# Optimization experiments

Measured on AMD Instinct MI355X. Metric: run time of the kernel, lower is better.

## Reference

```python
import jax, jax.numpy as jnp
import numpy as np

B, T, D = 4, 2048, 768
D_CONV, D_GRIF, D_FFN, K = 384, 384, 2048, 3
EPS = 1e-6


def rmsnorm(x, w):
    rms = jax.lax.rsqrt(jnp.mean(jnp.square(x.astype(jnp.float32)), axis=-1, keepdims=True) + EPS)
    return (x.astype(jnp.float32) * rms).astype(x.dtype) * w


def causal_dwconv(x, w):
    # x: [B,T,C], w: [C,K] depthwise causal conv
    k = w.shape[1]
    xp = jnp.pad(x, ((0, 0), (k - 1, 0), (0, 0)))  # left pad -> causal
    out = jax.lax.conv_general_dilated(
        xp.transpose(0, 2, 1), w[:, None, :],  # [B,C,T+K-1], [C,1,K]
        window_strides=(1,), padding='VALID',
        dimension_numbers=('NCW', 'OIW', 'NCW'),
        feature_group_count=w.shape[0])
    return out.transpose(0, 2, 1)  # [B,T,C]


def rg_lru(v, r, i, lam):
    # Griffin RG-LRU: log_a = -8*softplus(lam)*r; h_t = a*h_{t-1} + sqrt(1-a^2)*(i*v)
    log_a = -8.0 * jax.nn.softplus(lam) * r                # [B,T,Dg]
    a = jnp.exp(log_a)
    gated = jnp.sqrt(jnp.maximum(1.0 - jnp.exp(2.0 * log_a), EPS)) * (i * v)
    def comb(c1, c2):
        a1, b1 = c1
        a2, b2 = c2
        return (a1 * a2, a2 * b1 + b2)
    _, h = jax.lax.associative_scan(comb, (a, gated), axis=1)
    return h


def setup_inputs() -> dict:
    key = jax.random.key(0)
    ks = jax.random.split(key, 16)
    s_in = 1.0 / np.sqrt(D)
    s_ffn = 1.0 / np.sqrt(D_FFN)
    return {
        'x': jax.random.normal(ks[0], (B, T, D), jnp.float32),
        'velocity': jnp.zeros((B, T, D), jnp.float32),
        'pre_norm_w': jnp.ones((D,), jnp.float32),
        'conv_in_w': jax.random.normal(ks[1], (D, 2 * D_CONV), jnp.float32) * s_in,
        'conv_dw_w': jax.random.normal(ks[2], (D_CONV, K), jnp.float32) * (1.0 / np.sqrt(K)),
        'grif_v_w': jax.random.normal(ks[3], (D, D_GRIF), jnp.float32) * s_in,
        'grif_r_w': jax.random.normal(ks[4], (D, D_GRIF), jnp.float32) * s_in,
        'grif_i_w': jax.random.normal(ks[5], (D, D_GRIF), jnp.float32) * s_in,
        'grif_lam': jax.random.uniform(ks[6], (D_GRIF,), jnp.float32, 0.5, 2.0),
        'out_w': jax.random.normal(ks[7], (D, D), jnp.float32) * s_in,
        'log_beta': jnp.array(0.0, jnp.float32),  # log(0.5/(1-0.5))
        'ffn_norm_w': jnp.ones((D,), jnp.float32),
        'w1': jax.random.normal(ks[8], (D, D_FFN), jnp.float32) * s_in,
        'w3': jax.random.normal(ks[9], (D, D_FFN), jnp.float32) * s_in,
        'w2': jax.random.normal(ks[10], (D_FFN, D), jnp.float32) * s_ffn,
    }


def reference(x, velocity, pre_norm_w, conv_in_w, conv_dw_w, grif_v_w, grif_r_w,
              grif_i_w, grif_lam, out_w, log_beta, ffn_norm_w, w1, w3, w2):
    xn = rmsnorm(x, pre_norm_w)
    # GatedConv branch -> [B,T,D_CONV]
    u, g = jnp.split(xn @ conv_in_w, 2, axis=-1)
    conv_out = causal_dwconv(u, conv_dw_w) * jax.nn.silu(g)
    # Griffin RG-LRU branch -> [B,T,D_GRIF]
    v = xn @ grif_v_w
    r = jax.nn.sigmoid(xn @ grif_r_w)
    i = jax.nn.sigmoid(xn @ grif_i_w)
    griffin_out = rg_lru(v, r, i, grif_lam)
    # concat -> out_proj -> momentum residual
    mixer_out = jnp.concatenate([conv_out, griffin_out], axis=-1) @ out_w
    beta = jax.nn.sigmoid(log_beta)
    velocity = beta * velocity + mixer_out
    x = x + velocity
    # ffn: RMSNorm -> SwiGLU -> residual
    normed = rmsnorm(x, ffn_norm_w)
    x = x + (jax.nn.silu(normed @ w1) * (normed @ w3)) @ w2
    return (x, velocity)
```

## Files before the change

kernel.cpp:

```cpp
#include <hip/hip_runtime.h>
#include <hip/hip_bf16.h>
#include <cstdint>

#define BSZ   4
#define TSEQ  2048
#define DMOD  768
#define DCONV 384
#define DGRIF 384
#define DFFN  2048
#define BT    (BSZ*TSEQ)
#define NG1   1920
#define EPS_  1e-6f

typedef __bf16 bf16;
typedef __bf16 bf16x8 __attribute__((ext_vector_type(8)));
typedef float  f32x4  __attribute__((ext_vector_type(4)));

__device__ __forceinline__ float sigmoidf_(float x) { return 1.f / (1.f + __expf(-x)); }

__device__ __forceinline__ void gload_lds16(const void* g, void* l) {
  __builtin_amdgcn_global_load_lds(
      (const __attribute__((address_space(1))) void*)(uintptr_t)g,
      (__attribute__((address_space(3))) void*)(uint32_t)(uintptr_t)l,
      16, 0, 0);
}

__device__ __forceinline__ int swz_wg() {
  const int nwg = gridDim.x;
  const int bid = blockIdx.x;
  const int cpx = nwg >> 3;
  return (bid & 7) * cpx + (bid >> 3);
}

__global__ __launch_bounds__(256) void prep_kernel(
    const float* __restrict__ conv_in_w, const float* __restrict__ gv,
    const float* __restrict__ gr, const float* __restrict__ gi,
    const float* __restrict__ out_w, const float* __restrict__ w1,
    const float* __restrict__ w3, const float* __restrict__ w2,
    bf16* __restrict__ WT_G1, bf16* __restrict__ WT_OUT,
    bf16* __restrict__ WT_W13, bf16* __restrict__ WT_W2,
    const float* __restrict__ x, const float* __restrict__ pre_w,
    bf16* __restrict__ XN)
{
  __shared__ float tile[32][33];
  if (blockIdx.x >= 6624) {
    const int row = blockIdx.x - 6624;
    const int tid = threadIdx.x;
    const float* xr = x + (size_t)row * DMOD;
    float v0 = xr[tid], v1 = xr[tid + 256], v2 = xr[tid + 512];
    float s = v0*v0 + v1*v1 + v2*v2;
    #pragma unroll
    for (int o = 32; o > 0; o >>= 1) s += __shfl_down(s, o, 64);
    __shared__ float sbuf[4];
    if ((tid & 63) == 0) sbuf[tid >> 6] = s;
    __syncthreads();
    float tot = sbuf[0] + sbuf[1] + sbuf[2] + sbuf[3];
    float rms = rsqrtf(tot * (1.f / (float)DMOD) + EPS_);
    bf16* orow = XN + (size_t)row * DMOD;
    orow[tid]       = (bf16)(v0 * rms * pre_w[tid]);
    orow[tid + 256] = (bf16)(v1 * rms * pre_w[tid + 256]);
    orow[tid + 512] = (bf16)(v2 * rms * pre_w[tid + 512]);
    return;
  }
  int t = blockIdx.x;
  const float* W; bf16* Wt; int R, C, mode = 0, half = 0;
  if      (t < 576)  {           W = conv_in_w; Wt = WT_G1;                        R = 768;  C = 768; }
  else if (t < 864)  { t -= 576;  W = gv;  Wt = WT_G1 + (size_t)768  * DMOD;       R = 768;  C = 384; }
  else if (t < 1152) { t -= 864;  W = gr;  Wt = WT_G1 + (size_t)1152 * DMOD;       R = 768;  C = 384; }
  else if (t < 1440) { t -= 1152; W = gi;  Wt = WT_G1 + (size_t)1536 * DMOD;       R = 768;  C = 384; }
  else if (t < 2016) { t -= 1440; W = out_w; Wt = WT_OUT;                          R = 768;  C = 768; }
  else if (t < 3552) { t -= 2016; W = w1;  Wt = WT_W13; mode = 1; half = 0;        R = 768;  C = 2048; }
  else if (t < 5088) { t -= 3552; W = w3;  Wt = WT_W13; mode = 1; half = 64;       R = 768;  C = 2048; }
  else               { t -= 5088; W = w2;  Wt = WT_W2;                             R = 2048; C = 768; }

  const int xt = C >> 5;
  const int tc = (t % xt) * 32, tr = (t / xt) * 32;
  const int lx = threadIdx.x & 31;
  const int ly = threadIdx.x >> 5;
  #pragma unroll
  for (int i = ly; i < 32; i += 8) {
    int r = tr + i, c = tc + lx;
    tile[i][lx] = (r < R && c < C) ? W[(size_t)r * C + c] : 0.f;
  }
  __syncthreads();
  #pragma unroll
  for (int i = ly; i < 32; i += 8) {
    int oc = tc + i;
    int orr = tr + lx;
    if (oc < C && orr < R) {
      int orow = (mode == 0) ? oc : ((oc >> 6) << 7) + half + (oc & 63);
      Wt[(size_t)orow * R + orr] = (bf16)tile[lx][i];
    }
  }
}

__global__ __launch_bounds__(256) void rmsnorm_kernel(
    const float* __restrict__ x, const float* __restrict__ w, bf16* __restrict__ out)
{
  __shared__ float sbuf[4];
  const int row = blockIdx.x;
  const int tid = threadIdx.x;
  const float* xr = x + (size_t)row * DMOD;
  float v0 = xr[tid], v1 = xr[tid + 256], v2 = xr[tid + 512];
  float s = v0*v0 + v1*v1 + v2*v2;
  #pragma unroll
  for (int o = 32; o > 0; o >>= 1) s += __shfl_down(s, o, 64);
  if ((tid & 63) == 0) sbuf[tid >> 6] = s;
  __syncthreads();
  float tot = sbuf[0] + sbuf[1] + sbuf[2] + sbuf[3];
  float rms = rsqrtf(tot * (1.f / (float)DMOD) + EPS_);
  bf16* orow = out + (size_t)row * DMOD;
  orow[tid]       = (bf16)(v0 * rms * w[tid]);
  orow[tid + 256] = (bf16)(v1 * rms * w[tid + 256]);
  orow[tid + 512] = (bf16)(v2 * rms * w[tid + 512]);
}

__global__ __launch_bounds__(256) void gemm_w128d(
    const bf16* __restrict__ A, const bf16* __restrict__ Bt, bf16* __restrict__ C,
    int M, int N, int K, int nx)
{
  __shared__ alignas(16) unsigned short As[2][128 * 64];
  __shared__ alignas(16) unsigned short Bs[2][128 * 64];

  const int wg = swz_wg();
  const int m0 = (wg / nx) * 128, n0 = (wg % nx) * 128;
  const int tid  = threadIdx.x;
  const int wave = tid >> 6;
  const int lane = tid & 63;
  const int wr = wave >> 1, wc = wave & 1;

  f32x4 acc[4][4] = {};
  const int srow = lane >> 3;
  const int scol = ((lane & 7) ^ srow) * 8;
  const int lr = lane & 15;
  const int lsw = lr & 7;
  const int lk4 = lane >> 4;

  auto stage = [&](int buf, int k0) {
    #pragma unroll
    for (int it = 0; it < 4; ++it) {
      const int chunk = wave * 4 + it;
      const int row = chunk * 8 + srow;
      gload_lds16(A  + (size_t)(m0 + row) * K + k0 + scol, (char*)As[buf] + chunk * 1024);
      gload_lds16(Bt + (size_t)(n0 + row) * K + k0 + scol, (char*)Bs[buf] + chunk * 1024);
    }
  };

  stage(0, 0);
  __syncthreads();

  int cur = 0;
  for (int k0 = 0; k0 < K; k0 += 64) {
    if (k0 + 64 < K) stage(cur ^ 1, k0 + 64);
    #pragma unroll
    for (int kk = 0; kk < 2; ++kk) {
      bf16x8 af[4], bfr[4];
      #pragma unroll
      for (int i = 0; i < 4; ++i)
        af[i] = *reinterpret_cast<const bf16x8*>(
            &As[cur][(wr*64 + i*16 + lr) * 64 + (((kk*4 + lk4) ^ lsw) * 8)]);
      #pragma unroll
      for (int i = 0; i < 4; ++i)
        bfr[i] = *reinterpret_cast<const bf16x8*>(
            &Bs[cur][(wc*64 + i*16 + lr) * 64 + (((kk*4 + lk4) ^ lsw) * 8)]);
      #pragma unroll
      for (int mi = 0; mi < 4; ++mi)
        #pragma unroll
        for (int ni = 0; ni < 4; ++ni)
          acc[mi][ni] = __builtin_amdgcn_mfma_f32_16x16x32_bf16(af[mi], bfr[ni], acc[mi][ni], 0, 0, 0);
    }
    __syncthreads();
    cur ^= 1;
  }

  #pragma unroll
  for (int mi = 0; mi < 4; ++mi)
    #pragma unroll
    for (int ni = 0; ni < 4; ++ni)
      #pragma unroll
      for (int reg = 0; reg < 4; ++reg) {
        const int r = m0 + wr*64 + mi*16 + lk4 * 4 + reg;
        const int c = n0 + wc*64 + ni*16 + lr;
        C[(size_t)r * N + c] = (bf16)acc[mi][ni][reg];
      }
}

__global__ __launch_bounds__(256) void gemm_ffn13d(
    const bf16* __restrict__ A, const bf16* __restrict__ Bt, bf16* __restrict__ H,
    int M, int K)
{
  __shared__ alignas(16) unsigned short As[2][128 * 64];
  __shared__ alignas(16) unsigned short Bs[2][128 * 64];
  bf16* comb = reinterpret_cast<bf16*>(As);

  const int xcd = blockIdx.x & 7;
  const int w   = blockIdx.x >> 3;
  const int mt  = (xcd & 3) * 16 + (w >> 4);
  const int bx  = (xcd >> 2) * 16 + (w & 15);
  const int m0 = mt * 128;
  const int n0 = bx * 128;
  const int tid  = threadIdx.x;
  const int wave = tid >> 6;
  const int lane = tid & 63;
  const int wr = wave >> 1, wc = wave & 1;

  f32x4 acc[4][4] = {};
  const int srow = lane >> 3;
  const int scol = ((lane & 7) ^ srow) * 8;
  const int lr = lane & 15;
  const int lsw = lr & 7;
  const int lk4 = lane >> 4;

  auto stage = [&](int buf, int k0) {
    #pragma unroll
    for (int it = 0; it < 4; ++it) {
      const int chunk = wave * 4 + it;
      const int row = chunk * 8 + srow;
      gload_lds16(A  + (size_t)(m0 + row) * K + k0 + scol, (char*)As[buf] + chunk * 1024);
      gload_lds16(Bt + (size_t)(n0 + row) * K + k0 + scol, (char*)Bs[buf] + chunk * 1024);
    }
  };

  stage(0, 0);
  __syncthreads();

  int cur = 0;
  for (int k0 = 0; k0 < K; k0 += 64) {
    if (k0 + 64 < K) stage(cur ^ 1, k0 + 64);
    #pragma unroll
    for (int kk = 0; kk < 2; ++kk) {
      bf16x8 af[4], bfr[4];
      #pragma unroll
      for (int i = 0; i < 4; ++i)
        af[i] = *reinterpret_cast<const bf16x8*>(
            &As[cur][(wr*64 + i*16 + lr) * 64 + (((kk*4 + lk4) ^ lsw) * 8)]);
      #pragma unroll
      for (int i = 0; i < 4; ++i)
        bfr[i] = *reinterpret_cast<const bf16x8*>(
            &Bs[cur][(wc*64 + i*16 + lr) * 64 + (((kk*4 + lk4) ^ lsw) * 8)]);
      #pragma unroll
      for (int mi = 0; mi < 4; ++mi)
        #pragma unroll
        for (int ni = 0; ni < 4; ++ni)
          acc[mi][ni] = __builtin_amdgcn_mfma_f32_16x16x32_bf16(af[mi], bfr[ni], acc[mi][ni], 0, 0, 0);
    }
    __syncthreads();
    cur ^= 1;
  }

  if (wc == 1) {
    #pragma unroll
    for (int mi = 0; mi < 4; ++mi)
      #pragma unroll
      for (int ni = 0; ni < 4; ++ni)
        #pragma unroll
        for (int reg = 0; reg < 4; ++reg) {
          const int row = wr*64 + mi*16 + lk4 * 4 + reg;
          const int col = ni*16 + lr;
          comb[row * 64 + col] = (bf16)acc[mi][ni][reg];
        }
  }
  __syncthreads();
  if (wc == 0) {
    #pragma unroll
    for (int mi = 0; mi < 4; ++mi)
      #pragma unroll
      for (int ni = 0; ni < 4; ++ni)
        #pragma unroll
        for (int reg = 0; reg < 4; ++reg) {
          const int row = wr*64 + mi*16 + lk4 * 4 + reg;
          const int col = ni*16 + lr;
          float p3 = (float)comb[row * 64 + col];
          float p1 = acc[mi][ni][reg];
          H[(size_t)(m0 + row) * DFFN + bx * 64 + col] = (bf16)(p1 * sigmoidf_(p1) * p3);
        }
  }
}

template <int EPI>
__global__ __launch_bounds__(256) void gemm_n64(
    const bf16* __restrict__ A, const bf16* __restrict__ Bt, float* __restrict__ C,
    const float* __restrict__ xin, const float* __restrict__ vin,
    float* __restrict__ outv, const float* __restrict__ log_beta,
    int M, int N, int K, int nx)
{
  __shared__ alignas(16) unsigned short As[2][128 * 64];
  __shared__ alignas(16) unsigned short Bs[2][64 * 64];

  const int wg = swz_wg();
  const int m0 = (wg / nx) * 128, n0 = (wg % nx) * 64;
  const int tid  = threadIdx.x;
  const int wave = tid >> 6;
  const int lane = tid & 63;
  const int wr = wave >> 1, wc = wave & 1;

  f32x4 acc[4][2] = {};
  const int srow = lane >> 3;
  const int scol = ((lane & 7) ^ srow) * 8;
  const int lr = lane & 15;
  const int lsw = lr & 7;
  const int lk4 = lane >> 4;

  auto stage = [&](int buf, int k0) {
    #pragma unroll
    for (int it = 0; it < 6; ++it) {
      const int chunk = wave * 6 + it;
      if (chunk < 16) {
        const int row = chunk * 8 + srow;
        gload_lds16(A + (size_t)(m0 + row) * K + k0 + scol,
                    (char*)As[buf] + chunk * 1024);
      } else {
        const int row = (chunk - 16) * 8 + srow;
        gload_lds16(Bt + (size_t)(n0 + row) * K + k0 + scol,
                    (char*)Bs[buf] + (chunk - 16) * 1024);
      }
    }
  };

  stage(0, 0);
  __syncthreads();

  int cur = 0;
  for (int k0 = 0; k0 < K; k0 += 64) {
    if (k0 + 64 < K) stage(cur ^ 1, k0 + 64);
    #pragma unroll
    for (int kk = 0; kk < 2; ++kk) {
      bf16x8 af[4], bfr[2];
      #pragma unroll
      for (int i = 0; i < 4; ++i)
        af[i] = *reinterpret_cast<const bf16x8*>(
            &As[cur][(wr*64 + i*16 + lr) * 64 + (((kk*4 + lk4) ^ lsw) * 8)]);
      #pragma unroll
      for (int i = 0; i < 2; ++i)
        bfr[i] = *reinterpret_cast<const bf16x8*>(
            &Bs[cur][(wc*32 + i*16 + lr) * 64 + (((kk*4 + lk4) ^ lsw) * 8)]);
      #pragma unroll
      for (int mi = 0; mi < 4; ++mi)
        #pragma unroll
        for (int ni = 0; ni < 2; ++ni)
          acc[mi][ni] = __builtin_amdgcn_mfma_f32_16x16x32_bf16(af[mi], bfr[ni], acc[mi][ni], 0, 0, 0);
    }
    __syncthreads();
    cur ^= 1;
  }

  const float beta = (EPI == 0) ? sigmoidf_(log_beta[0]) : 0.f;
  #pragma unroll
  for (int mi = 0; mi < 4; ++mi)
    #pragma unroll
    for (int ni = 0; ni < 2; ++ni)
      #pragma unroll
      for (int reg = 0; reg < 4; ++reg) {
        const int r = m0 + wr*64 + mi*16 + lk4 * 4 + reg;
        const int c = n0 + wc*32 + ni*16 + lr;
        const size_t off = (size_t)r * N + c;
        float v = acc[mi][ni][reg];
        if (EPI == 0) {
          float vel = beta * vin[off] + v;
          float x1  = xin[off] + vel;
          outv[off] = vel;
          C[off] = x1;
        } else {
          C[off] += v;
        }
      }
}

#define NCH  32
#define CLEN 64

__device__ __forceinline__ void lru_step(const bf16* row, int c, float coef,
                                         float& a, float& g)
{
  float v  = (float)row[2*DCONV + c];
  float r  = sigmoidf_((float)row[2*DCONV + DGRIF + c]);
  float is = sigmoidf_((float)row[2*DCONV + 2*DGRIF + c]);
  float la = coef * r;
  a = __expf(la);
  g = sqrtf(fmaxf(1.f - __expf(2.f * la), EPS_)) * (is * v);
}

__global__ __launch_bounds__(256) void lru_pass1(
    const bf16* __restrict__ g1, const float* __restrict__ lam,
    float* __restrict__ cA, float* __restrict__ cB)
{
  const int idx = blockIdx.x * 256 + threadIdx.x;
  const int c = idx % DGRIF;
  const int rest = idx / DGRIF;
  const int j = rest & (NCH - 1);
  const int b = rest / NCH;
  const float coef = -8.f * log1pf(__expf(lam[c]));
  const bf16* base = g1 + (size_t)(b * TSEQ + j * CLEN) * NG1;
  float A = 1.f, Bv = 0.f;
  #pragma unroll 4
  for (int t = 0; t < CLEN; ++t) {
    float a, g;
    lru_step(base + (size_t)t * NG1, c, coef, a, g);
    A *= a;
    Bv = a * Bv + g;
  }
  cA[((size_t)b * DGRIF + c) * NCH + j] = A;
  cB[((size_t)b * DGRIF + c) * NCH + j] = Bv;
}

__global__ __launch_bounds__(256) void lru_pass2(
    const bf16* __restrict__ g1, const float* __restrict__ lam,
    const float* __restrict__ cA, const float* __restrict__ cB,
    const float* __restrict__ dw, bf16* __restrict__ mixin)
{
  const int idx = blockIdx.x * 256 + threadIdx.x;
  const int c = idx % DGRIF;
  const int rest = idx / DGRIF;
  const int j = rest & (NCH - 1);
  const int b = rest / NCH;
  const float coef = -8.f * log1pf(__expf(lam[c]));
  float Hc = 0.f;
  const float* pa = cA + ((size_t)b * DGRIF + c) * NCH;
  const float* pb = cB + ((size_t)b * DGRIF + c) * NCH;
  for (int k = 0; k < j; ++k) Hc = pa[k] * Hc + pb[k];

  const int t0 = j * CLEN;
  const bf16* base = g1 + (size_t)(b * TSEQ + t0) * NG1;
  const float w0 = dw[c*3], w1 = dw[c*3 + 1], w2 = dw[c*3 + 2];
  float u1 = (t0 >= 1) ? (float)base[-(ptrdiff_t)NG1 + c]     : 0.f;
  float u0 = (t0 >= 2) ? (float)base[-(ptrdiff_t)(2*NG1) + c] : 0.f;

  bf16* mbase = mixin + (size_t)(b * TSEQ + t0) * DMOD;
  #pragma unroll 4
  for (int t = 0; t < CLEN; ++t) {
    const bf16* row = base + (size_t)t * NG1;
    float u2 = (float)row[c];
    float gg = (float)row[DCONV + c];
    float conv = u0 * w0 + u1 * w1 + u2 * w2;
    mbase[(size_t)t * DMOD + c] = (bf16)(conv * (gg * sigmoidf_(gg)));
    u0 = u1; u1 = u2;
    float a, g;
    lru_step(row, c, coef, a, g);
    Hc = a * Hc + g;
    mbase[(size_t)t * DMOD + DCONV + c] = (bf16)Hc;
  }
}

extern "C" void kernel_launch(void* const* d_in, const int* in_sizes, int n_in,
                              void* d_out, int out_size, void* d_ws, size_t ws_size,
                              hipStream_t stream)
{
  const float* x         = (const float*)d_in[0];
  const float* vel_in    = (const float*)d_in[1];
  const float* pre_w     = (const float*)d_in[2];
  const float* conv_in_w = (const float*)d_in[3];
  const float* conv_dw   = (const float*)d_in[4];
  const float* gv        = (const float*)d_in[5];
  const float* gr        = (const float*)d_in[6];
  const float* gi        = (const float*)d_in[7];
  const float* lam       = (const float*)d_in[8];
  const float* out_w     = (const float*)d_in[9];
  const float* log_beta  = (const float*)d_in[10];
  const float* ffn_w     = (const float*)d_in[11];
  const float* w1        = (const float*)d_in[12];
  const float* w3        = (const float*)d_in[13];
  const float* w2        = (const float*)d_in[14];

  char* ws = (char*)d_ws;
  size_t off = 0;
  auto alloc = [&](size_t bytes) { void* p = ws + off; off += (bytes + 255) & ~(size_t)255; return p; };

  bf16*  WT_G1  = (bf16*)alloc((size_t)NG1 * DMOD * 2);
  bf16*  WT_OUT = (bf16*)alloc((size_t)DMOD * DMOD * 2);
  bf16*  WT_W13 = (bf16*)alloc((size_t)2 * DFFN * DMOD * 2);
  bf16*  WT_W2  = (bf16*)alloc((size_t)DMOD * DFFN * 2);
  float* CA     = (float*)alloc((size_t)BSZ * DGRIF * NCH * 4);
  float* CB     = (float*)alloc((size_t)BSZ * DGRIF * NCH * 4);
  bf16*  XN     = (bf16*)alloc((size_t)BT * DMOD * 2);
  bf16*  G1     = (bf16*)alloc((size_t)BT * NG1 * 2);
  bf16*  MIXIN  = (bf16*)alloc((size_t)BT * DMOD * 2);
  bf16*  H      = (bf16*)alloc((size_t)BT * DFFN * 2);
  bf16*  NORMED = (bf16*)alloc((size_t)BT * DMOD * 2);

  float* OUTX   = (float*)d_out;
  float* OUTV   = OUTX + (size_t)BT * DMOD;

  prep_kernel<<<6624 + BT, 256, 0, stream>>>(conv_in_w, gv, gr, gi, out_w, w1, w3, w2,
                                             WT_G1, WT_OUT, WT_W13, WT_W2,
                                             x, pre_w, XN);

  gemm_w128d<<<(NG1/128) * (BT/128), 256, 0, stream>>>(XN, WT_G1, G1, BT, NG1, DMOD, NG1/128);

  lru_pass1<<<(BSZ * NCH * DGRIF) / 256, 256, 0, stream>>>(G1, lam, CA, CB);
  lru_pass2<<<(BSZ * NCH * DGRIF) / 256, 256, 0, stream>>>(G1, lam, CA, CB, conv_dw, MIXIN);

  gemm_n64<0><<<(DMOD/64) * (BT/128), 256, 0, stream>>>(MIXIN, WT_OUT, OUTX, x, vel_in, OUTV,
                                                        log_beta, BT, DMOD, DMOD, DMOD/64);

  rmsnorm_kernel<<<BT, 256, 0, stream>>>(OUTX, ffn_w, NORMED);

  gemm_ffn13d<<<(BT/128) * (DFFN/64), 256, 0, stream>>>(NORMED, WT_W13, H, BT, DMOD);

  gemm_n64<1><<<(DMOD/64) * (BT/128), 256, 0, stream>>>(H, WT_W2, OUTX, nullptr, nullptr, nullptr,
                                                        nullptr, BT, DMOD, DFFN, DMOD/64);
}
```

Before: 248.1 us.

## Triple-buffer B tiles in FFN13 GEMM and vectorize LRU over channel pairs

Measured after the change: 273.4 us. 10.2% more time.

```diff
diff --git a/kernel.cpp b/kernel.cpp
--- a/kernel.cpp
+++ b/kernel.cpp
@@ -13,6 +13,7 @@
 #define EPS_  1e-6f
 
 typedef __bf16 bf16;
+typedef __bf16 bf16x2 __attribute__((ext_vector_type(2)));
 typedef __bf16 bf16x8 __attribute__((ext_vector_type(8)));
 typedef float  f32x4  __attribute__((ext_vector_type(4)));
 
@@ -31,6 +32,10 @@
   const int cpx = nwg >> 3;
   return (bid & 7) * cpx + (bid >> 3);
 }
+
+#define VM4() asm volatile("s_waitcnt vmcnt(4)" ::: "memory")
+#define VM0() asm volatile("s_waitcnt vmcnt(0)" ::: "memory")
+#define SBAR() __builtin_amdgcn_s_barrier()
 
 __global__ __launch_bounds__(256) void prep_kernel(
     const float* __restrict__ conv_in_w, const float* __restrict__ gv,
@@ -185,12 +190,12 @@
       }
 }
 
-__global__ __launch_bounds__(256) void gemm_ffn13d(
+__global__ __launch_bounds__(256) void gemm_ffn13e(
     const bf16* __restrict__ A, const bf16* __restrict__ Bt, bf16* __restrict__ H,
     int M, int K)
 {
   __shared__ alignas(16) unsigned short As[2][128 * 64];
-  __shared__ alignas(16) unsigned short Bs[2][128 * 64];
+  __shared__ alignas(16) unsigned short Bs[3][128 * 64];
   bf16* comb = reinterpret_cast<bf16*>(As);
 
   const int xcd = blockIdx.x & 7;
@@ -211,41 +216,54 @@
   const int lsw = lr & 7;
   const int lk4 = lane >> 4;
 
-  auto stage = [&](int buf, int k0) {
+  auto stageA = [&](int buf, int t) {
+    const int k0 = t * 64;
     #pragma unroll
     for (int it = 0; it < 4; ++it) {
       const int chunk = wave * 4 + it;
       const int row = chunk * 8 + srow;
-      gload_lds16(A  + (size_t)(m0 + row) * K + k0 + scol, (char*)As[buf] + chunk * 1024);
+      gload_lds16(A + (size_t)(m0 + row) * K + k0 + scol, (char*)As[buf] + chunk * 1024);
+    }
+  };
+  auto stageB = [&](int buf, int t) {
+    const int k0 = t * 64;
+    #pragma unroll
+    for (int it = 0; it < 4; ++it) {
+      const int chunk = wave * 4 + it;
+      const int row = chunk * 8 + srow;
       gload_lds16(Bt + (size_t)(n0 + row) * K + k0 + scol, (char*)Bs[buf] + chunk * 1024);
     }
   };
 
-  stage(0, 0);
-  __syncthreads();
-
-  int cur = 0;
-  for (int k0 = 0; k0 < K; k0 += 64) {
-    if (k0 + 64 < K) stage(cur ^ 1, k0 + 64);
+  const int nt = K >> 6;
+  stageA(0, 0); stageB(0, 0);
+  if (nt > 1) { stageB(1, 1); VM4(); } else { VM0(); }
+  SBAR();
+
+  for (int t = 0; t < nt; ++t) {
+    if (t + 1 < nt) stageA((t + 1) & 1, t + 1);
+    if (t + 2 < nt) stageB((t + 2) % 3, t + 2);
+    const int ca = t & 1;
+    const int cb = t % 3;
     #pragma unroll
     for (int kk = 0; kk < 2; ++kk) {
       bf16x8 af[4], bfr[4];
       #pragma unroll
       for (int i = 0; i < 4; ++i)
         af[i] = *reinterpret_cast<const bf16x8*>(
-            &As[cur][(wr*64 + i*16 + lr) * 64 + (((kk*4 + lk4) ^ lsw) * 8)]);
+            &As[ca][(wr*64 + i*16 + lr) * 64 + (((kk*4 + lk4) ^ lsw) * 8)]);
       #pragma unroll
       for (int i = 0; i < 4; ++i)
         bfr[i] = *reinterpret_cast<const bf16x8*>(
-            &Bs[cur][(wc*64 + i*16 + lr) * 64 + (((kk*4 + lk4) ^ lsw) * 8)]);
+            &Bs[cb][(wc*64 + i*16 + lr) * 64 + (((kk*4 + lk4) ^ lsw) * 8)]);
       #pragma unroll
       for (int mi = 0; mi < 4; ++mi)
         #pragma unroll
         for (int ni = 0; ni < 4; ++ni)
           acc[mi][ni] = __builtin_amdgcn_mfma_f32_16x16x32_bf16(af[mi], bfr[ni], acc[mi][ni], 0, 0, 0);
     }
-    __syncthreads();
-    cur ^= 1;
+    if (t + 2 < nt) { VM4(); } else { VM0(); }
+    SBAR();
   }
 
   if (wc == 1) {
@@ -366,18 +384,22 @@
       }
 }
 
-#define NCH  32
-#define CLEN 64
-
-__device__ __forceinline__ void lru_step(const bf16* row, int c, float coef,
-                                         float& a, float& g)
-{
-  float v  = (float)row[2*DCONV + c];
-  float r  = sigmoidf_((float)row[2*DCONV + DGRIF + c]);
-  float is = sigmoidf_((float)row[2*DCONV + 2*DGRIF + c]);
-  float la = coef * r;
-  a = __expf(la);
-  g = sqrtf(fmaxf(1.f - __expf(2.f * la), EPS_)) * (is * v);
+#define NCH  64
+#define CLEN 32
+#define CPB  192
+
+__device__ __forceinline__ void lru_step2(const bf16* row, int c2,
+    float coef0, float coef1, float& a0, float& g0, float& a1, float& g1)
+{
+  bf16x2 v  = *reinterpret_cast<const bf16x2*>(row + 2*DCONV + c2);
+  bf16x2 r  = *reinterpret_cast<const bf16x2*>(row + 2*DCONV + DGRIF + c2);
+  bf16x2 ii = *reinterpret_cast<const bf16x2*>(row + 2*DCONV + 2*DGRIF + c2);
+  float la0 = coef0 * sigmoidf_((float)r[0]);
+  float la1 = coef1 * sigmoidf_((float)r[1]);
+  a0 = __expf(la0);
+  a1 = __expf(la1);
+  g0 = sqrtf(fmaxf(1.f - __expf(2.f * la0), EPS_)) * (sigmoidf_((float)ii[0]) * (float)v[0]);
+  g1 = sqrtf(fmaxf(1.f - __expf(2.f * la1), EPS_)) * (sigmoidf_((float)ii[1]) * (float)v[1]);
 }
 
 __global__ __launch_bounds__(256) void lru_pass1(
@@ -385,22 +407,26 @@
     float* __restrict__ cA, float* __restrict__ cB)
 {
   const int idx = blockIdx.x * 256 + threadIdx.x;
-  const int c = idx % DGRIF;
-  const int rest = idx / DGRIF;
+  const int cp = idx % CPB;
+  const int rest = idx / CPB;
   const int j = rest & (NCH - 1);
-  const int b = rest / NCH;
-  const float coef = -8.f * log1pf(__expf(lam[c]));
+  const int b = rest >> 6;
+  const int c2 = cp * 2;
+  const float coef0 = -8.f * log1pf(__expf(lam[c2]));
+  const float coef1 = -8.f * log1pf(__expf(lam[c2 + 1]));
   const bf16* base = g1 + (size_t)(b * TSEQ + j * CLEN) * NG1;
-  float A = 1.f, Bv = 0.f;
+  float A0 = 1.f, Bv0 = 0.f, A1 = 1.f, Bv1 = 0.f;
   #pragma unroll 4
   for (int t = 0; t < CLEN; ++t) {
-    float a, g;
-    lru_step(base + (size_t)t * NG1, c, coef, a, g);
-    A *= a;
-    Bv = a * Bv + g;
-  }
-  cA[((size_t)b * DGRIF + c) * NCH + j] = A;
-  cB[((size_t)b * DGRIF + c) * NCH + j] = Bv;
+    float a0, g0, a1, g1v;
+    lru_step2(base + (size_t)t * NG1, c2, coef0, coef1, a0, g0, a1, g1v);
+    A0 *= a0; Bv0 = a0 * Bv0 + g0;
+    A1 *= a1; Bv1 = a1 * Bv1 + g1v;
+  }
+  cA[((size_t)b * DGRIF + c2) * NCH + j]     = A0;
+  cA[((size_t)b * DGRIF + c2 + 1) * NCH + j] = A1;
+  cB[((size_t)b * DGRIF + c2) * NCH + j]     = Bv0;
+  cB[((size_t)b * DGRIF + c2 + 1) * NCH + j] = Bv1;
 }
 
 __global__ __launch_bounds__(256) void lru_pass2(
@@ -409,35 +435,60 @@
     const float* __restrict__ dw, bf16* __restrict__ mixin)
 {
   const int idx = blockIdx.x * 256 + threadIdx.x;
-  const int c = idx % DGRIF;
-  const int rest = idx / DGRIF;
+  const int cp = idx % CPB;
+  const int rest = idx / CPB;
   const int j = rest & (NCH - 1);
-  const int b = rest / NCH;
-  const float coef = -8.f * log1pf(__expf(lam[c]));
-  float Hc = 0.f;
-  const float* pa = cA + ((size_t)b * DGRIF + c) * NCH;
-  const float* pb = cB + ((size_t)b * DGRIF + c) * NCH;
-  for (int k = 0; k < j; ++k) Hc = pa[k] * Hc + pb[k];
+  const int b = rest >> 6;
+  const int c2 = cp * 2;
+  const float coef0 = -8.f * log1pf(__expf(lam[c2]));
+  const float coef1 = -8.f * log1pf(__expf(lam[c2 + 1]));
+  float Hc0 = 0.f, Hc1 = 0.f;
+  const float* pa0 = cA + ((size_t)b * DGRIF + c2) * NCH;
+  const float* pb0 = cB + ((size_t)b * DGRIF + c2) * NCH;
+  const float* pa1 = pa0 + NCH;
+  const float* pb1 = pb0 + NCH;
+  for (int k = 0; k < j; ++k) {
+    Hc0 = pa0[k] * Hc0 + pb0[k];
+    Hc1 = pa1[k] * Hc1 + pb1[k];
+  }
 
   const int t0 = j * CLEN;
   const bf16* base = g1 + (size_t)(b * TSEQ + t0) * NG1;
-  const float w0 = dw[c*3], w1 = dw[c*3 + 1], w2 = dw[c*3 + 2];
-  float u1 = (t0 >= 1) ? (float)base[-(ptrdiff_t)NG1 + c]     : 0.f;
-  float u0 = (t0 >= 2) ? (float)base[-(ptrdiff_t)(2*NG1) + c] : 0.f;
+  const float w00 = dw[c2*3], w01 = dw[c2*3 + 1], w02 = dw[c2*3 + 2];
+  const float w10 = dw[c2*3 + 3], w11 = dw[c2*3 + 4], w12 = dw[c2*3 + 5];
+  float u1a = 0.f, u1b = 0.f, u0a = 0.f, u0b = 0.f;
+  if (t0 >= 1) {
+    bf16x2 p = *reinterpret_cast<const bf16x2*>(base - (ptrdiff_t)NG1 + c2);
+    u1a = (float)p[0]; u1b = (float)p[1];
+  }
+  if (t0 >= 2) {
+    bf16x2 p = *reinterpret_cast<const bf16x2*>(base - (ptrdiff_t)(2*NG1) + c2);
+    u0a = (float)p[0]; u0b = (float)p[1];
+  }
 
   bf16* mbase = mixin + (size_t)(b * TSEQ + t0) * DMOD;
   #pragma unroll 4
   for (int t = 0; t < CLEN; ++t) {
     const bf16* row = base + (size_t)t * NG1;
-    float u2 = (float)row[c];
-    float gg = (float)row[DCONV + c];
-    float conv = u0 * w0 + u1 * w1 + u2 * w2;
-    mbase[(size_t)t * DMOD + c] = (bf16)(conv * (gg * sigmoidf_(gg)));
-    u0 = u1; u1 = u2;
-    float a, g;
-    lru_step(row, c, coef, a, g);
-    Hc = a * Hc + g;
-    mbase[(size_t)t * DMOD + DCONV + c] = (bf16)Hc;
+    bf16x2 u2 = *reinterpret_cast<const bf16x2*>(row + c2);
+    bf16x2 gg = *reinterpret_cast<const bf16x2*>(row + DCONV + c2);
+    float conv0 = u0a * w00 + u1a * w01 + (float)u2[0] * w02;
+    float conv1 = u0b * w10 + u1b * w11 + (float)u2[1] * w12;
+    float g0f = (float)gg[0], g1f = (float)gg[1];
+    bf16x2 cw;
+    cw[0] = (bf16)(conv0 * (g0f * sigmoidf_(g0f)));
+    cw[1] = (bf16)(conv1 * (g1f * sigmoidf_(g1f)));
+    *reinterpret_cast<bf16x2*>(mbase + (size_t)t * DMOD + c2) = cw;
+    u0a = u1a; u1a = (float)u2[0];
+    u0b = u1b; u1b = (float)u2[1];
+    float a0, g0, a1, g1v;
+    lru_step2(row, c2, coef0, coef1, a0, g0, a1, g1v);
+    Hc0 = a0 * Hc0 + g0;
+    Hc1 = a1 * Hc1 + g1v;
+    bf16x2 hw;
+    hw[0] = (bf16)Hc0;
+    hw[1] = (bf16)Hc1;
+    *reinterpret_cast<bf16x2*>(mbase + (size_t)t * DMOD + DCONV + c2) = hw;
   }
 }
 
@@ -486,15 +537,15 @@
 
   gemm_w128d<<<(NG1/128) * (BT/128), 256, 0, stream>>>(XN, WT_G1, G1, BT, NG1, DMOD, NG1/128);
 
-  lru_pass1<<<(BSZ * NCH * DGRIF) / 256, 256, 0, stream>>>(G1, lam, CA, CB);
-  lru_pass2<<<(BSZ * NCH * DGRIF) / 256, 256, 0, stream>>>(G1, lam, CA, CB, conv_dw, MIXIN);
+  lru_pass1<<<(BSZ * NCH * CPB) / 256, 256, 0, stream>>>(G1, lam, CA, CB);
+  lru_pass2<<<(BSZ * NCH * CPB) / 256, 256, 0, stream>>>(G1, lam, CA, CB, conv_dw, MIXIN);
 
   gemm_n64<0><<<(DMOD/64) * (BT/128), 256, 0, stream>>>(MIXIN, WT_OUT, OUTX, x, vel_in, OUTV,
                                                         log_beta, BT, DMOD, DMOD, DMOD/64);
 
   rmsnorm_kernel<<<BT, 256, 0, stream>>>(OUTX, ffn_w, NORMED);
 
-  gemm_ffn13d<<<(BT/128) * (DFFN/64), 256, 0, stream>>>(NORMED, WT_W13, H, BT, DMOD);
+  gemm_ffn13e<<<(BT/128) * (DFFN/64), 256, 0, stream>>>(NORMED, WT_W13, H, BT, DMOD);
 
   gemm_n64<1><<<(DMOD/64) * (BT/128), 256, 0, stream>>>(H, WT_W2, OUTX, nullptr, nullptr, nullptr,
                                                         nullptr, BT, DMOD, DFFN, DMOD/64);
```
